# Optimization experiments

Hardware: AMD Instinct MI355X
Metric: run time of the kernel (lower is better)

Reference implementation:

```python
import jax, jax.numpy as jnp
import numpy as np

B, S, D, C = 2, 4096, 768, 8192
SCALE = 1.0
LN_EPS = 1e-5


def setup_inputs() -> dict:
    key = jax.random.key(0)
    ks = jax.random.split(key, 8)
    std = 0.03
    return {
        "x": jax.random.normal(ks[0], (B, S, D), dtype=jnp.float32),
        "attention_masks": jax.random.randint(ks[1], (B, S), 0, 2).astype(jnp.int32),
        "Wk": jax.random.normal(ks[2], (D, D), dtype=jnp.float32) * std,
        "Wv": jax.random.normal(ks[3], (D, D), dtype=jnp.float32) * std,
        "bv": jnp.zeros((D,), dtype=jnp.float32),
        "Q": jax.random.normal(ks[4], (C, D), dtype=jnp.float32) * std,  # label_representations
        "ln_gamma": jnp.ones((D,), dtype=jnp.float32),
        "ln_beta": jnp.zeros((D,), dtype=jnp.float32),
        "w_out": jax.random.normal(ks[5], (D,), dtype=jnp.float32) * std,  # output_linear.weight [1, D]
        "b_out": jnp.zeros((), dtype=jnp.float32),  # output_linear.bias [1]
    }


def reference(x, attention_masks, Wk, Wv, bv, Q, ln_gamma, ln_beta, w_out, b_out):
    # K, V projections (torch Linear: x @ W.T + b)
    K = jnp.einsum("bsd,ed->bse", x, Wk)
    V = jnp.einsum("bsd,ed->bse", x, Wv) + bv
    # label-query cross-attention scores: [B, C, S]
    scores = jnp.einsum("cd,bsd->bcs", Q, K)
    # additive mask: -inf where attention_masks == 0 (intended semantics of pad/repeat/masked_fill)
    scores = jnp.where(attention_masks[:, None, :] == 0, -jnp.inf, scores)
    attn = jax.nn.softmax(scores / SCALE, axis=2)  # [B, C, S]
    y = jnp.einsum("bcs,bsd->bcd", attn, V)  # [B, C, D]
    # LayerNorm over last dim
    mu = jnp.mean(y, axis=-1, keepdims=True)
    var = jnp.mean((y - mu) ** 2, axis=-1, keepdims=True)
    y = (y - mu) * jax.lax.rsqrt(var + LN_EPS) * ln_gamma + ln_beta
    # elementwise weight-mul-sum output head: [B, C]
    return jnp.einsum("bcd,d->bc", y, w_out) + b_out
```

## Files before the change

### kernel.cpp

```cpp
#include <hip/hip_runtime.h>
#include <hip/hip_bf16.h>
#include <hip/hip_fp16.h>

typedef _Float16 f16x8 __attribute__((ext_vector_type(8)));
typedef _Float16 f16x4 __attribute__((ext_vector_type(4)));
typedef float f32x4 __attribute__((ext_vector_type(4)));

#define AS1 __attribute__((address_space(1)))
#define AS3 __attribute__((address_space(3)))
#define MFMA16(a, b, c) __builtin_amdgcn_mfma_f32_16x16x32_f16(a, b, c, 0, 0, 0)
#define BARRIER asm volatile("s_barrier" ::: "memory")

#define LDP 2304

__global__ __launch_bounds__(256) void maskscan(const int* __restrict__ am,
                                                int* __restrict__ idx,
                                                int* __restrict__ meta) {
  const int b = blockIdx.x, t = threadIdx.x;
  const int* m = am + (size_t)b * 4096;
  int* ix = idx + (size_t)b * 4096;
  __shared__ int cnt[256];
  __shared__ int pre[257];
  int loc[16], c = 0;
#pragma unroll
  for (int j = 0; j < 16; ++j) {
    loc[j] = m[t * 16 + j];
    c += (loc[j] != 0);
  }
  cnt[t] = c;
  __syncthreads();
  if (t == 0) {
    pre[0] = 0;
    for (int i = 0; i < 256; ++i) pre[i + 1] = pre[i] + cnt[i];
  }
  __syncthreads();
  int p = pre[t];
#pragma unroll
  for (int j = 0; j < 16; ++j)
    if (loc[j]) ix[p++] = t * 16 + j;
  const int valid = pre[256];
  int nsp = ((valid + 255) >> 8) << 8;
  if (nsp < 512) nsp = 512;
  for (int j = valid + t; j < nsp; j += 256) ix[j] = -1;
  if (t == 0) { meta[2 * b] = valid; meta[2 * b + 1] = nsp; }
}

__global__ __launch_bounds__(192) void gather_cvt(const float* __restrict__ x,
                                                  const int* __restrict__ idx,
                                                  const int* __restrict__ meta,
                                                  unsigned short* __restrict__ xc) {
  const int b = blockIdx.y, row = blockIdx.x, t = threadIdx.x;
  if (row >= meta[2 * b + 1]) return;
  const int src = idx[(size_t)b * 4096 + row];
  unsigned short* dst = xc + ((size_t)b * 4096 + row) * 768 + t * 4;
  f16x4 h;
  if (src < 0) {
    h[0] = h[1] = h[2] = h[3] = (_Float16)0.0f;
  } else {
    float4 v = *(const float4*)(x + ((size_t)b * 4096 + src) * 768 + t * 4);
    h[0] = (_Float16)v.x; h[1] = (_Float16)v.y; h[2] = (_Float16)v.z; h[3] = (_Float16)v.w;
  }
  *(f16x4*)dst = h;
}

__global__ __launch_bounds__(256) void cvt_f32_f16(const float* __restrict__ in,
                                                   unsigned short* __restrict__ out,
                                                   int n8) {
  int i = blockIdx.x * 256 + threadIdx.x;
  if (i >= n8) return;
  const float4* p = (const float4*)in + 2 * (size_t)i;
  float4 a = p[0], b = p[1];
  f16x8 h;
  h[0] = (_Float16)a.x; h[1] = (_Float16)a.y; h[2] = (_Float16)a.z; h[3] = (_Float16)a.w;
  h[4] = (_Float16)b.x; h[5] = (_Float16)b.y; h[6] = (_Float16)b.z; h[7] = (_Float16)b.w;
  *(f16x8*)(out + (size_t)i * 8) = h;
}

template <int OMODE, bool RBIAS, int EXITD>
__global__ __launch_bounds__(256) void gemm_nt(const unsigned short* __restrict__ A, int lda,
                                               const unsigned short* __restrict__ B, int ldb,
                                               void* __restrict__ Cout, int ldc,
                                               const float* __restrict__ bias,
                                               const int* __restrict__ meta,
                                               int N, int K) {
  const int nbn = N >> 7;
  const int bm = blockIdx.x / nbn, bn = blockIdx.x % nbn;
  if constexpr (EXITD == 1) {
    if (((bm & 31) << 7) >= meta[2 * (bm >> 5) + 1]) return;
  } else if constexpr (EXITD == 2) {
    if (((bn & 31) << 7) >= meta[2 * (bn >> 5) + 1]) return;
  }
  __shared__ __attribute__((aligned(16))) unsigned short As[128 * 64];
  __shared__ __attribute__((aligned(16))) unsigned short Bs[128 * 64];
  const int tid = threadIdx.x;
  const int w = tid >> 6, l = tid & 63;
  const int wr = w >> 1, wc = w & 1;
  const int lr = l & 15, lg = l >> 4;

  const unsigned short* Ab = A + (size_t)bm * 128 * lda;
  const unsigned short* Bb = B + (size_t)bn * 128 * ldb;

  f32x4 acc[4][4] = {};

  auto ldfrag = [&](const unsigned short* base, int row, int kk) {
    int off = row * 128 + kk * 64 + lg * 16;
    off ^= (row & 7) << 4;
    return *(const f16x8*)((const unsigned char*)base + off);
  };

  for (int kt = 0; kt < K; kt += 64) {
#pragma unroll
    for (int i = 0; i < 4; ++i) {
      const int c = i * 256 + w * 64 + l;
      const int row = c >> 3, col = (((c & 7) ^ (row & 7)) << 3);
      __builtin_amdgcn_global_load_lds((const AS1 void*)(Ab + (size_t)row * lda + kt + col),
                                       (AS3 void*)(As + (i * 256 + w * 64) * 8), 16, 0, 0);
    }
#pragma unroll
    for (int i = 0; i < 4; ++i) {
      const int c = i * 256 + w * 64 + l;
      const int row = c >> 3, col = (((c & 7) ^ (row & 7)) << 3);
      __builtin_amdgcn_global_load_lds((const AS1 void*)(Bb + (size_t)row * ldb + kt + col),
                                       (AS3 void*)(Bs + (i * 256 + w * 64) * 8), 16, 0, 0);
    }
    __syncthreads();
#pragma unroll
    for (int kk = 0; kk < 2; ++kk) {
      f16x8 af[4], bf[4];
#pragma unroll
      for (int mi = 0; mi < 4; ++mi) af[mi] = ldfrag(As, wr * 64 + mi * 16 + lr, kk);
#pragma unroll
      for (int ni = 0; ni < 4; ++ni) bf[ni] = ldfrag(Bs, wc * 64 + ni * 16 + lr, kk);
#pragma unroll
      for (int mi = 0; mi < 4; ++mi)
#pragma unroll
        for (int ni = 0; ni < 4; ++ni)
          acc[mi][ni] = MFMA16(af[mi], bf[ni], acc[mi][ni]);
    }
    __syncthreads();
  }

#pragma unroll
  for (int mi = 0; mi < 4; ++mi) {
#pragma unroll
    for (int r = 0; r < 4; ++r) {
      const int row = bm * 128 + wr * 64 + mi * 16 + lg * 4 + r;
      const float badd = RBIAS ? bias[row] : 0.0f;
#pragma unroll
      for (int ni = 0; ni < 4; ++ni) {
        const int col = bn * 128 + wc * 64 + ni * 16 + lr;
        float v = acc[mi][ni][r] + badd;
        if constexpr (OMODE == 0)
          ((unsigned short*)Cout)[(size_t)row * ldc + col] =
              __builtin_bit_cast(unsigned short, (_Float16)v);
        else
          ((float*)Cout)[(size_t)row * ldc + col] = v;
      }
    }
  }
}

template <int EPI>
__global__ __launch_bounds__(512, 1) void gemm256(
    const unsigned short* __restrict__ A, int lda, size_t sAz,
    const unsigned short* __restrict__ B, int ldb, size_t sBz,
    unsigned short* __restrict__ Cout, int ldc, size_t sCz, size_t sCk,
    const int* __restrict__ meta, int NTfix) {
  __shared__ __attribute__((aligned(16))) unsigned char lds[131072];
  const int tid = threadIdx.x;
  const int wv = tid >> 6, l = tid & 63;
  const int wm = wv >> 2, wn = wv & 3;
  const int lr = l & 15, lg = l >> 4;
  const int bid = blockIdx.x;

  const int xr = ((lr >> 1) & 3) << 4;
  const int aoff = ((wm * 128 + lr) << 6) + ((lg << 4) ^ xr);
  const int boff = ((wn * 64 + lr) << 6) + ((lg << 4) ^ xr);

  const unsigned short* Abase = nullptr;
  const unsigned short* Bbase = nullptr;

  auto stage = [&](int uu) {
    const int tau = uu >> 2, r = uu & 3;
    const int regionOff = ((tau & 1) << 16) | ((r & 1) << 15) | ((r >> 1) << 14);
    const unsigned short* base = (r & 1) ? Bbase : Abase;
    const int ld = (r & 1) ? ldb : lda;
    const int kcol0 = tau * 64 + ((r >> 1) << 5);
#pragma unroll
    for (int j = 0; j < 2; ++j) {
      const int row = wv * 32 + j * 16 + (l >> 2);
      const int col = kcol0 + ((((l & 3) ^ ((row >> 1) & 3))) << 3);
      __builtin_amdgcn_global_load_lds(
          (const AS1 void*)(base + (size_t)row * ld + col),
          (AS3 void*)(lds + regionOff + wv * 2048 + j * 1024), 16, 0, 0);
    }
  };

  constexpr int NPASS = (EPI == 2) ? 2 : 1;

  for (int pass = 0; pass < NPASS; ++pass) {
    int z, bm, bn, NT, koff, ks = 0;
    if constexpr (EPI == 2) {
      if (pass == 0) {
        z = bid >> 8;
        const int rem = bid & 255;
        bm = rem & 31;
        bn = rem >> 5;
        if (bn * 256 >= meta[2 * z + 1]) continue;
      } else {
        const int tn0 = max(0, (meta[1] >> 8) - 8);
        const int tn1 = max(0, (meta[3] >> 8) - 8);
        if (bid >= 32 * (tn0 + tn1)) break;
        int t = bid;
        if (t < 32 * tn0) { z = 0; }
        else { t -= 32 * tn0; z = 1; }
        bm = t & 31;
        bn = 8 + (t >> 5);
      }
      NT = NTfix;
      koff = 0;
    } else {
      z = bid / 192;
      const int r = bid - z * 192;
      ks = r / 96;
      const int q = r - ks * 96;
      bm = q & 31;
      bn = q >> 5;
      const int nsp = meta[2 * z + 1];
      NT = nsp >> 7;
      koff = ks * (nsp >> 1);
    }
    const int valid = meta[2 * z];

    Abase = A + (size_t)z * sAz + koff + (size_t)bm * 256 * lda;
    Bbase = B + (size_t)z * sBz + koff + (size_t)bn * 256 * ldb;

    const int NT4 = NT * 4;
    f32x4 acc[8][4] = {};
    f16x8 Ar0[4], Ar1[4], Br0[4], Br1[4];

    auto rdA4 = [&](f16x8* d, int mh, int kk, int bo) {
#pragma unroll
      for (int i = 0; i < 4; ++i)
        d[i] = *(const f16x8*)(lds + bo + (kk << 14) + aoff + (4 * mh + i) * 1024);
    };
    auto rdB4 = [&](f16x8* d, int kk, int bo) {
#pragma unroll
      for (int i = 0; i < 4; ++i)
        d[i] = *(const f16x8*)(lds + 32768 + bo + (kk << 14) + boff + i * 1024);
    };
    auto mm16 = [&](const f16x8* Aq, const f16x8* Bq, int mh) {
#pragma unroll
      for (int i = 0; i < 4; ++i)
#pragma unroll
        for (int j = 0; j < 4; ++j)
          acc[4 * mh + i][j] = MFMA16(Aq[i], Bq[j], acc[4 * mh + i][j]);
    };

    for (int i = 0; i < 6; ++i) stage(i);
    int u = 6;
    asm volatile("s_waitcnt vmcnt(4)" ::: "memory");
    BARRIER;
    rdA4(Ar0, 0, 0, 0);
    rdB4(Br0, 0, 0);

    for (int t = 0; t < NT; ++t) {
      const int bo = (t & 1) << 16;
      const int bo2 = bo ^ 65536;
      if (u < NT4) stage(u);
      ++u;
      __builtin_amdgcn_s_setprio(1);
      rdA4(Ar1, 1, 0, bo);
      mm16(Ar0, Br0, 0);
      __builtin_amdgcn_s_setprio(0);
      BARRIER;
      if (u < NT4) stage(u);
      ++u;
      __builtin_amdgcn_s_setprio(1);
      rdA4(Ar0, 0, 1, bo);
      rdB4(Br1, 1, bo);
      mm16(Ar1, Br0, 1);
      __builtin_amdgcn_s_setprio(0);
      BARRIER;
      if (u < NT4) stage(u);
      ++u;
      __builtin_amdgcn_s_setprio(1);
      rdA4(Ar1, 1, 1, bo);
      mm16(Ar0, Br1, 0);
      __builtin_amdgcn_s_setprio(0);
      if (t + 2 < NT) {
        asm volatile("s_waitcnt vmcnt(2)" ::: "memory");
      } else if (t + 2 == NT) {
        asm volatile("s_waitcnt vmcnt(0)" ::: "memory");
      }
      BARRIER;
      if (u < NT4) stage(u);
      ++u;
      __builtin_amdgcn_s_setprio(1);
      if (t + 1 < NT) {
        rdA4(Ar0, 0, 0, bo2);
        rdB4(Br0, 0, bo2);
      }
      mm16(Ar1, Br1, 1);
      __builtin_amdgcn_s_setprio(0);
      BARRIER;
    }

    const size_t crow0 = (size_t)bm * 256 + wm * 128;
    const int ccol0 = bn * 256 + wn * 64;
    unsigned short* Cz = Cout + (size_t)z * sCz + (size_t)ks * sCk;
#pragma unroll
    for (int mf = 0; mf < 8; ++mf) {
#pragma unroll
      for (int rr = 0; rr < 4; ++rr) {
        const size_t rb = (crow0 + mf * 16 + lg * 4 + rr) * (size_t)ldc;
#pragma unroll
        for (int nf = 0; nf < 4; ++nf) {
          const int col = ccol0 + nf * 16 + lr;
          float v = acc[mf][nf][rr];
          if constexpr (EPI == 2) v = (col < valid) ? __expf(v) : 0.0f;
          Cz[rb + col] = __builtin_bit_cast(unsigned short, (_Float16)v);
        }
      }
    }
  }
}

__device__ inline float block_sum(float v, float* sh, int t) {
#pragma unroll
  for (int o = 32; o; o >>= 1) v += __shfl_xor(v, o);
  __syncthreads();
  if ((t & 63) == 0) sh[t >> 6] = v;
  __syncthreads();
  return sh[0] + sh[1] + sh[2] + sh[3];
}

__global__ __launch_bounds__(256) void ln_head(const unsigned short* __restrict__ yp,
                                               size_t zoff, size_t koff,
                                               const float* __restrict__ gam,
                                               const float* __restrict__ bet,
                                               const float* __restrict__ wo,
                                               const float* __restrict__ bo,
                                               float* __restrict__ out) {
  const int z = blockIdx.y;
  const size_t rbase = (size_t)z * zoff + (size_t)blockIdx.x * 768;
  const _Float16* y0 = (const _Float16*)yp + rbase;
  const _Float16* y1 = y0 + koff;
  const int t = threadIdx.x;
  float a0 = (float)y0[t] + (float)y1[t];
  float a1 = (float)y0[t + 256] + (float)y1[t + 256];
  float a2 = (float)y0[t + 512] + (float)y1[t + 512];
  __shared__ float sh[4];
  float s = block_sum(a0 + a1 + a2, sh, t);
  float mu = s * (1.0f / 768.0f);
  float d0 = a0 - mu, d1 = a1 - mu, d2 = a2 - mu;
  float q = block_sum(d0 * d0 + d1 * d1 + d2 * d2, sh, t);
  float rs = rsqrtf(q * (1.0f / 768.0f) + 1e-5f);
  float o = (d0 * rs * gam[t] + bet[t]) * wo[t] +
            (d1 * rs * gam[t + 256] + bet[t + 256]) * wo[t + 256] +
            (d2 * rs * gam[t + 512] + bet[t + 512]) * wo[t + 512];
  o = block_sum(o, sh, t);
  if (t == 0) out[(size_t)z * 8192 + blockIdx.x] = o + bo[0];
}

extern "C" void kernel_launch(void* const* d_in, const int* in_sizes, int n_in,
                              void* d_out, int out_size, void* d_ws, size_t ws_size,
                              hipStream_t stream) {
  const float* x  = (const float*)d_in[0];
  const int*   am = (const int*)d_in[1];
  const float* Wk = (const float*)d_in[2];
  const float* Wv = (const float*)d_in[3];
  const float* bv = (const float*)d_in[4];
  const float* Q  = (const float*)d_in[5];
  const float* gam = (const float*)d_in[6];
  const float* bet = (const float*)d_in[7];
  const float* wo  = (const float*)d_in[8];
  const float* bo  = (const float*)d_in[9];
  float* out = (float*)d_out;

  const int S = 4096, D = 768, C = 8192;
  const size_t nX = (size_t)2 * S * D;
  const size_t nW = (size_t)D * D;
  const size_t nQ = (size_t)C * D;
  const size_t nPc = (size_t)C * LDP;
  const size_t nY = (size_t)C * D;

  unsigned short* xc  = (unsigned short*)d_ws;
  unsigned short* Wkb = xc + nX;
  unsigned short* Wvb = Wkb + nW;
  unsigned short* Qb  = Wvb + nW;
  unsigned short* Kb  = Qb + nQ;
  unsigned short* Vt  = Kb + nX;
  unsigned short* P   = Vt + nX;
  unsigned short* yp  = P + 2 * nPc;
  int* idx  = (int*)(yp + 4 * nY);
  int* meta = idx + 2 * 4096;

  maskscan<<<2, 256, 0, stream>>>(am, idx, meta);
  gather_cvt<<<dim3(4096, 2), 192, 0, stream>>>(x, idx, meta, xc);

  cvt_f32_f16<<<(int)(nW / 8 / 256), 256, 0, stream>>>(Wk, Wkb, (int)(nW / 8));
  cvt_f32_f16<<<(int)(nW / 8 / 256), 256, 0, stream>>>(Wv, Wvb, (int)(nW / 8));
  cvt_f32_f16<<<(int)(nQ / 8 / 256), 256, 0, stream>>>(Q, Qb, (int)(nQ / 8));

  gemm_nt<0, false, 1><<<(8192 / 128) * (768 / 128), 256, 0, stream>>>(
      xc, D, Wkb, D, Kb, D, nullptr, meta, 768, D);
  gemm_nt<0, true, 2><<<(768 / 128) * (8192 / 128), 256, 0, stream>>>(
      Wvb, D, xc, D, Vt, 2 * S, bv, meta, 2 * S, D);

  gemm256<2><<<dim3(512, 1), 512, 0, stream>>>(
      Qb, D, 0, Kb, D, (size_t)S * D, P, LDP, nPc, 0, meta, 12);

  gemm256<0><<<dim3(384, 1), 512, 0, stream>>>(
      P, LDP, nPc, Vt, 2 * S, (size_t)S, yp, D, 2 * nY, nY, meta, 0);

  ln_head<<<dim3(C, 2), 256, 0, stream>>>(yp, 2 * nY, nY, gam, bet, wo, bo, out);
}
```

Before: 224.7 us.

## Restructure GEMM main loop into ping-pong phases with sched barriers

Rewrites the inner GEMM loop so each phase first issues its LDS fragment reads and the next global stage, then hits a barrier, then runs an MFMA cluster fenced by sched_barrier. Register double-buffering of A/B fragments is dropped in favour of a single A buffer plus two B buffers, and the vmcnt wait depths are changed to match a deeper in-flight load count. This aims for a cleaner alternation of memory and MFMA work across waves and lower VGPR pressure. The cost is extra barriers per iteration and no overlap of LDS reads with MFMA inside a wave.

```diff
diff --git a/kernel.cpp b/kernel.cpp
--- a/kernel.cpp
+++ b/kernel.cpp
@@ -10,6 +10,10 @@
 #define AS3 __attribute__((address_space(3)))
 #define MFMA16(a, b, c) __builtin_amdgcn_mfma_f32_16x16x32_f16(a, b, c, 0, 0, 0)
 #define BARRIER asm volatile("s_barrier" ::: "memory")
+#define SCHED0 __builtin_amdgcn_sched_barrier(0)
+#define VM8 asm volatile("s_waitcnt vmcnt(8)" ::: "memory")
+#define VM4 asm volatile("s_waitcnt vmcnt(4)" ::: "memory")
+#define VM0 asm volatile("s_waitcnt vmcnt(0)" ::: "memory")
 
 #define LDP 2304
 
@@ -237,7 +241,7 @@
 
     const int NT4 = NT * 4;
     f32x4 acc[8][4] = {};
-    f16x8 Ar0[4], Ar1[4], Br0[4], Br1[4];
+    f16x8 Aq[4], Bq0[4], Bq1[4];
 
     auto rdA4 = [&](f16x8* d, int mh, int kk, int bo) {
 #pragma unroll
@@ -249,60 +253,65 @@
       for (int i = 0; i < 4; ++i)
         d[i] = *(const f16x8*)(lds + 32768 + bo + (kk << 14) + boff + i * 1024);
     };
-    auto mm16 = [&](const f16x8* Aq, const f16x8* Bq, int mh) {
+    auto mm16 = [&](const f16x8* Av, const f16x8* Bv, int mh) {
 #pragma unroll
       for (int i = 0; i < 4; ++i)
 #pragma unroll
         for (int j = 0; j < 4; ++j)
-          acc[4 * mh + i][j] = MFMA16(Aq[i], Bq[j], acc[4 * mh + i][j]);
+          acc[4 * mh + i][j] = MFMA16(Av[i], Bv[j], acc[4 * mh + i][j]);
     };
 
     for (int i = 0; i < 6; ++i) stage(i);
     int u = 6;
-    asm volatile("s_waitcnt vmcnt(4)" ::: "memory");
+    VM8;
     BARRIER;
-    rdA4(Ar0, 0, 0, 0);
-    rdB4(Br0, 0, 0);
 
     for (int t = 0; t < NT; ++t) {
       const int bo = (t & 1) << 16;
-      const int bo2 = bo ^ 65536;
+      rdA4(Aq, 0, 0, bo);
+      rdB4(Bq0, 0, bo);
       if (u < NT4) stage(u);
       ++u;
+      BARRIER;
+      SCHED0;
       __builtin_amdgcn_s_setprio(1);
-      rdA4(Ar1, 1, 0, bo);
-      mm16(Ar0, Br0, 0);
+      mm16(Aq, Bq0, 0);
       __builtin_amdgcn_s_setprio(0);
-      BARRIER;
+      SCHED0;
+      BARRIER;
+      rdA4(Aq, 1, 0, bo);
       if (u < NT4) stage(u);
       ++u;
+      BARRIER;
+      SCHED0;
       __builtin_amdgcn_s_setprio(1);
-      rdA4(Ar0, 0, 1, bo);
-      rdB4(Br1, 1, bo);
-      mm16(Ar1, Br0, 1);
+      mm16(Aq, Bq0, 1);
       __builtin_amdgcn_s_setprio(0);
-      BARRIER;
+      SCHED0;
+      if (t + 1 < NT) VM8; else VM0;
+      BARRIER;
+      rdA4(Aq, 0, 1, bo);
+      rdB4(Bq1, 1, bo);
       if (u < NT4) stage(u);
       ++u;
+      BARRIER;
+      SCHED0;
       __builtin_amdgcn_s_setprio(1);
-      rdA4(Ar1, 1, 1, bo);
-      mm16(Ar0, Br1, 0);
+      mm16(Aq, Bq1, 0);
       __builtin_amdgcn_s_setprio(0);
-      if (t + 2 < NT) {
-        asm volatile("s_waitcnt vmcnt(2)" ::: "memory");
-      } else if (t + 2 == NT) {
-        asm volatile("s_waitcnt vmcnt(0)" ::: "memory");
-      }
-      BARRIER;
+      SCHED0;
+      BARRIER;
+      rdA4(Aq, 1, 1, bo);
       if (u < NT4) stage(u);
       ++u;
+      BARRIER;
+      SCHED0;
       __builtin_amdgcn_s_setprio(1);
-      if (t + 1 < NT) {
-        rdA4(Ar0, 0, 0, bo2);
-        rdB4(Br0, 0, bo2);
-      }
-      mm16(Ar1, Br1, 1);
+      mm16(Aq, Bq1, 1);
       __builtin_amdgcn_s_setprio(0);
+      SCHED0;
+      if (t + 2 < NT) VM8;
+      else if (t + 2 == NT) VM4;
       BARRIER;
     }
 
```

Result: slower. 230.3 us (+2.5%).
